# Optimization experiments

Hardware: AMD Instinct MI355X
Metric: run time of the kernel (lower is better)

Reference implementation:

```python
import jax, jax.numpy as jnp
import numpy as np

T, B, S, D, H, E, F, K = 1024, 4, 1024, 1024, 16, 8, 2048, 2


def layer_norm(x, g, b, eps=1e-5):
    mu = x.mean(-1, keepdims=True)
    var = ((x - mu) ** 2).mean(-1, keepdims=True)
    return (x - mu) * jax.lax.rsqrt(var + eps) * g + b


def mha(q_in, k_in, v_in, Wq, bq, Wk, bk, Wv, bv, Wo, bo, n_heads, mask):
    # q_in: [Lq,B,D], k_in/v_in: [Lk,B,D]
    Lq, Bb, Dd = q_in.shape
    Lk = k_in.shape[0]
    hd = Dd // n_heads
    scale = 1.0 / np.sqrt(hd)
    q = ((q_in @ Wq + bq) * scale).reshape(Lq, Bb, n_heads, hd)
    k = (k_in @ Wk + bk).reshape(Lk, Bb, n_heads, hd)
    v = (v_in @ Wv + bv).reshape(Lk, Bb, n_heads, hd)
    scores = jnp.einsum('qbhd,kbhd->bhqk', q, k)  # [B,H,Lq,Lk]
    if mask is not None:
        scores = scores + mask  # additive mask broadcast over B,H
    p = jax.nn.softmax(scores, axis=-1)
    o = jnp.einsum('bhqk,kbhd->qbhd', p, v).reshape(Lq, Bb, Dd)
    return o @ Wo + bo


def moe_ffn(x2, gate_W, W1, b1, W2, b2, top_k):
    # x2: [N,D] flattened tokens. Top-k routing: softmax over the k selected logits.
    logits = x2 @ gate_W                      # [N,E]
    top_v, top_i = jax.lax.top_k(logits, top_k)
    gk = jax.nn.softmax(top_v, axis=-1)       # [N,k]
    gates = jnp.sum(jax.nn.one_hot(top_i, logits.shape[-1], dtype=x2.dtype) * gk[..., None], axis=1)  # [N,E] sparse
    out = jnp.zeros_like(x2)
    for e in range(W1.shape[0]):  # fixed small expert count
        h = jax.nn.relu(x2 @ W1[e] + b1[e])   # [N,F]
        out = out + gates[:, e:e + 1] * (h @ W2[e] + b2[e])
    return out


def _forward(x, encoder_out, self_attn_mask,
             ln1_g, ln1_b, ln2_g, ln2_b, ln3_g, ln3_b,
             sa_Wq, sa_bq, sa_Wk, sa_bk, sa_Wv, sa_bv, sa_Wo, sa_bo,
             ca_Wq, ca_bq, ca_Wk, ca_bk, ca_Wv, ca_bv, ca_Wo, ca_bo,
             gate_W, moe_W1, moe_b1, moe_W2, moe_b2):
    # pre-LN self-attention
    res = x
    xn = layer_norm(x, ln1_g, ln1_b)
    a = mha(xn, xn, xn, sa_Wq, sa_bq, sa_Wk, sa_bk, sa_Wv, sa_bv, sa_Wo, sa_bo, H, self_attn_mask)
    x = res + a
    # pre-LN cross-attention
    res = x
    xn = layer_norm(x, ln2_g, ln2_b)
    a = mha(xn, encoder_out, encoder_out, ca_Wq, ca_bq, ca_Wk, ca_bk, ca_Wv, ca_bv, ca_Wo, ca_bo, H, None)
    x = res + a
    # pre-LN MoE FFN
    res = x
    xn = layer_norm(x, ln3_g, ln3_b)
    m = moe_ffn(xn.reshape(-1, D), gate_W, moe_W1, moe_b1, moe_W2, moe_b2, K).reshape(x.shape)
    return res + m


def setup_inputs() -> dict:
    key = jax.random.key(0)
    ks = jax.random.split(key, 20)
    w = lambda k, shp: (jax.random.normal(k, shp, jnp.float32) * 0.02)
    causal = jnp.where(jnp.arange(T)[:, None] >= jnp.arange(T)[None, :], 0.0, -1e9).astype(jnp.float32)
    return {
        'x': jax.random.normal(ks[0], (T, B, D), jnp.float32),
        'encoder_out': jax.random.normal(ks[1], (S, B, D), jnp.float32),
        'self_attn_mask': causal,
        'ln1_g': jnp.ones((D,), jnp.float32), 'ln1_b': jnp.zeros((D,), jnp.float32),
        'ln2_g': jnp.ones((D,), jnp.float32), 'ln2_b': jnp.zeros((D,), jnp.float32),
        'ln3_g': jnp.ones((D,), jnp.float32), 'ln3_b': jnp.zeros((D,), jnp.float32),
        'sa_Wq': w(ks[2], (D, D)), 'sa_bq': jnp.zeros((D,), jnp.float32),
        'sa_Wk': w(ks[3], (D, D)), 'sa_bk': jnp.zeros((D,), jnp.float32),
        'sa_Wv': w(ks[4], (D, D)), 'sa_bv': jnp.zeros((D,), jnp.float32),
        'sa_Wo': w(ks[5], (D, D)), 'sa_bo': jnp.zeros((D,), jnp.float32),
        'ca_Wq': w(ks[6], (D, D)), 'ca_bq': jnp.zeros((D,), jnp.float32),
        'ca_Wk': w(ks[7], (D, D)), 'ca_bk': jnp.zeros((D,), jnp.float32),
        'ca_Wv': w(ks[8], (D, D)), 'ca_bv': jnp.zeros((D,), jnp.float32),
        'ca_Wo': w(ks[9], (D, D)), 'ca_bo': jnp.zeros((D,), jnp.float32),
        'gate_W': w(ks[10], (D, E)),
        'moe_W1': w(ks[11], (E, D, F)), 'moe_b1': jnp.zeros((E, F), jnp.float32),
        'moe_W2': w(ks[12], (E, F, D)), 'moe_b2': jnp.zeros((E, D), jnp.float32),
    }


def reference(x, encoder_out, self_attn_mask,
              ln1_g, ln1_b, ln2_g, ln2_b, ln3_g, ln3_b,
              sa_Wq, sa_bq, sa_Wk, sa_bk, sa_Wv, sa_bv, sa_Wo, sa_bo,
              ca_Wq, ca_bq, ca_Wk, ca_bk, ca_Wv, ca_bv, ca_Wo, ca_bo,
              gate_W, moe_W1, moe_b1, moe_W2, moe_b2):
    return _forward(x, encoder_out, self_attn_mask,
                    ln1_g, ln1_b, ln2_g, ln2_b, ln3_g, ln3_b,
                    sa_Wq, sa_bq, sa_Wk, sa_bk, sa_Wv, sa_bv, sa_Wo, sa_bo,
                    ca_Wq, ca_bq, ca_Wk, ca_bk, ca_Wv, ca_bv, ca_Wo, ca_bo,
                    gate_W, moe_W1, moe_b1, moe_W2, moe_b2)
```

## Files before the change

### kernel.cpp

```cpp
#include <hip/hip_runtime.h>
#include <hip/hip_bf16.h>

typedef unsigned short u16;
typedef float f32x4 __attribute__((ext_vector_type(4)));
typedef __bf16 bf16x8 __attribute__((ext_vector_type(8)));
typedef unsigned short u16x8 __attribute__((ext_vector_type(8)));
typedef unsigned short u16x4 __attribute__((ext_vector_type(4)));

__device__ __forceinline__ u16 f2bf(float f) {
    unsigned int u = __builtin_bit_cast(unsigned int, f);
    u += 0x7fffu + ((u >> 16) & 1u);
    return (u16)(u >> 16);
}
__device__ __forceinline__ float bf2f(u16 h) {
    unsigned int u = ((unsigned int)h) << 16;
    return __builtin_bit_cast(float, u);
}
__device__ __forceinline__ f32x4 mfma_bf16(u16x8 a, u16x8 b, f32x4 c) {
    return __builtin_amdgcn_mfma_f32_16x16x32_bf16(
        __builtin_bit_cast(bf16x8, a), __builtin_bit_cast(bf16x8, b), c, 0, 0, 0);
}
__device__ __forceinline__ void gload16(const void* g, void* l) {
    __builtin_amdgcn_global_load_lds(
        (const __attribute__((address_space(1))) unsigned int*)g,
        (__attribute__((address_space(3))) unsigned int*)l, 16, 0, 0);
}
__device__ __forceinline__ int swz_bid(int hw, int nwg) {
    return (hw & 7) * (nwg >> 3) + (hw >> 3);
}

template<bool GATHER>
__device__ __forceinline__ void gemm_core(
        const u16* __restrict__ Ab, const u16* __restrict__ Bb,
        int m0, int n0, int Klen, int Ksa, int Ksb, int cnt, const int* __restrict__ idx,
        u16* lds_a, u16* lds_b, f32x4 (&acc)[4][4]) {
    const int tid = threadIdx.x;
    const int w = tid >> 6, l = tid & 63;
    const int c8 = l & 7, r8 = l >> 3;
    const int lr = l & 15, lg = l >> 4;
    const int wr = (w >> 1) * 64, wc = (w & 1) * 64;
    const int swz = (c8 ^ r8) << 4;

    const char* asrc[4];
    const char* bsrc[4];
    #pragma unroll
    for (int i = 0; i < 4; i++) {
        int row = w * 32 + i * 8 + r8;
        int gr = m0 + row; if (gr > cnt - 1) gr = cnt - 1;
        if (GATHER) gr = idx[gr];
        asrc[i] = (const char*)Ab + (size_t)gr * Ksa * 2 + swz;
        bsrc[i] = (const char*)Bb + (size_t)(n0 + row) * Ksb * 2 + swz;
    }
    for (int k0 = 0; k0 < Klen; k0 += 64) {
        __syncthreads();
        #pragma unroll
        for (int i = 0; i < 4; i++) {
            gload16(asrc[i] + (size_t)k0 * 2, lds_a + (w * 32 + i * 8) * 64);
            gload16(bsrc[i] + (size_t)k0 * 2, lds_b + (w * 32 + i * 8) * 64);
        }
        __syncthreads();
        #pragma unroll
        for (int kk = 0; kk < 2; kk++) {
            u16x8 af[4], bfr[4];
            #pragma unroll
            for (int mi = 0; mi < 4; mi++) {
                int m = wr + mi * 16 + lr;
                af[mi] = *(const u16x8*)((const char*)lds_a + m * 128 + (((kk * 4 + lg) ^ (m & 7)) << 4));
            }
            #pragma unroll
            for (int ni = 0; ni < 4; ni++) {
                int n = wc + ni * 16 + lr;
                bfr[ni] = *(const u16x8*)((const char*)lds_b + n * 128 + (((kk * 4 + lg) ^ (n & 7)) << 4));
            }
            #pragma unroll
            for (int mi = 0; mi < 4; mi++)
                #pragma unroll
                for (int ni = 0; ni < 4; ni++)
                    acc[mi][ni] = mfma_bf16(af[mi], bfr[ni], acc[mi][ni]);
        }
    }
}

struct Slab5 { const u16* a; const u16* bt; const float* bias; u16* cb; float sc; };
struct Slabs5 { Slab5 s[5]; };

template<int MODE, int NSLAB>
__global__ __launch_bounds__(256, 3) void gemm_dense(
        Slabs5 P, const float* __restrict__ extra, float* __restrict__ Cf, int K) {
    __shared__ __align__(16) u16 lds_a[128 * 64];
    __shared__ __align__(16) u16 lds_b[128 * 64];
    const int gx = NSLAB * 8;
    const int lid = swz_bid((int)blockIdx.x + gx * (int)blockIdx.y, gx * 32);
    const int bx = lid % gx, by = lid / gx;
    const int slab = (NSLAB == 1) ? 0 : (bx >> 3);
    const int n0 = ((NSLAB == 1) ? bx : (bx & 7)) * 128;
    const int m0 = by * 128;
    f32x4 acc[4][4];
    #pragma unroll
    for (int i = 0; i < 4; i++)
        #pragma unroll
        for (int j = 0; j < 4; j++) acc[i][j] = (f32x4){0.f, 0.f, 0.f, 0.f};

    gemm_core<false>(P.s[slab].a, P.s[slab].bt, m0, n0, K, K, K, 0x7fffffff, nullptr, lds_a, lds_b, acc);

    const int tid = threadIdx.x, w = tid >> 6, l = tid & 63;
    const int lr = l & 15, lg = l >> 4, wr = (w >> 1) * 64, wc = (w & 1) * 64;
    const float* bias = P.s[slab].bias;
    #pragma unroll
    for (int ni = 0; ni < 4; ni++) {
        int col = n0 + wc + ni * 16 + lr;
        float bv = bias[col];
        #pragma unroll
        for (int mi = 0; mi < 4; mi++) {
            #pragma unroll
            for (int r = 0; r < 4; r++) {
                int row = m0 + wr + mi * 16 + lg * 4 + r;
                float v = acc[mi][ni][r] + bv;
                size_t off = (size_t)row * 1024 + col;
                if (MODE == 1) Cf[off] = v + extra[off];
                else           P.s[slab].cb[off] = f2bf(v * P.s[slab].sc);
            }
        }
    }
}

__global__ __launch_bounds__(256, 3) void gemm_moe1(
        const u16* __restrict__ XNb, const u16* __restrict__ W1b, const float* __restrict__ b1,
        u16* __restrict__ HB, const int* __restrict__ eidx,
        const int* __restrict__ ecnt, const int* __restrict__ eoff) {
    __shared__ __align__(16) u16 lds_a[128 * 64];
    __shared__ __align__(16) u16 lds_b[128 * 64];
    const int lid = swz_bid((int)blockIdx.x + 16 * ((int)blockIdx.y + 32 * (int)blockIdx.z), 4096);
    const int bx = lid & 15, rem = lid >> 4;
    const int by = rem & 31, e = rem >> 5;
    const int cnt = ecnt[e];
    const int m0 = by * 128;
    if (m0 >= cnt) return;
    const int n0 = bx * 128;
    const int* idx = eidx + e * 4096;
    f32x4 acc[4][4];
    #pragma unroll
    for (int i = 0; i < 4; i++)
        #pragma unroll
        for (int j = 0; j < 4; j++) acc[i][j] = (f32x4){0.f, 0.f, 0.f, 0.f};

    gemm_core<true>(XNb, W1b + (size_t)e * 2048 * 1024, m0, n0, 1024, 1024, 1024, cnt, idx, lds_a, lds_b, acc);

    const int tid = threadIdx.x, w = tid >> 6, l = tid & 63;
    const int lr = l & 15, lg = l >> 4, wr = (w >> 1) * 64, wc = (w & 1) * 64;
    u16* H = HB + (size_t)eoff[e] * 2048;
    const float* bias = b1 + (size_t)e * 2048;
    #pragma unroll
    for (int ni = 0; ni < 4; ni++) {
        int col = n0 + wc + ni * 16 + lr;
        float bv = bias[col];
        #pragma unroll
        for (int mi = 0; mi < 4; mi++) {
            #pragma unroll
            for (int r = 0; r < 4; r++) {
                int row = m0 + wr + mi * 16 + lg * 4 + r;
                if (row < cnt)
                    H[(size_t)row * 2048 + col] = f2bf(fmaxf(acc[mi][ni][r] + bv, 0.f));
            }
        }
    }
}

__global__ __launch_bounds__(256, 3) void gemm_moe2(
        const u16* __restrict__ HB, const u16* __restrict__ W2b, const float* __restrict__ b2,
        u16* __restrict__ Y,
        const int* __restrict__ ecnt, const int* __restrict__ eoff) {
    __shared__ __align__(16) u16 lds_a[128 * 64];
    __shared__ __align__(16) u16 lds_b[128 * 64];
    const int lid = swz_bid((int)blockIdx.x + 8 * ((int)blockIdx.y + 32 * (int)blockIdx.z), 2048);
    const int bx = lid & 7, rem = lid >> 3;
    const int by = rem & 31, e = rem >> 5;
    const int cnt = ecnt[e];
    const int m0 = by * 128;
    if (m0 >= cnt) return;
    const int n0 = bx * 128;
    const u16* Ae = HB + (size_t)eoff[e] * 2048;
    f32x4 acc[4][4];
    #pragma unroll
    for (int i = 0; i < 4; i++)
        #pragma unroll
        for (int j = 0; j < 4; j++) acc[i][j] = (f32x4){0.f, 0.f, 0.f, 0.f};

    gemm_core<false>(Ae, W2b + (size_t)e * 1024 * 2048, m0, n0, 2048, 2048, 2048, cnt, nullptr, lds_a, lds_b, acc);

    const int tid = threadIdx.x, w = tid >> 6, l = tid & 63;
    const int lr = l & 15, lg = l >> 4, wr = (w >> 1) * 64, wc = (w & 1) * 64;
    const float* bias = b2 + (size_t)e * 1024;
    u16* Ye = Y + (size_t)eoff[e] * 1024;
    #pragma unroll
    for (int ni = 0; ni < 4; ni++) {
        int col = n0 + wc + ni * 16 + lr;
        float bv = bias[col];
        #pragma unroll
        for (int mi = 0; mi < 4; mi++) {
            #pragma unroll
            for (int r = 0; r < 4; r++) {
                int row = m0 + wr + mi * 16 + lg * 4 + r;
                if (row < cnt)
                    Ye[(size_t)row * 1024 + col] = f2bf(acc[mi][ni][r] + bv);
            }
        }
    }
}

__global__ void combine_kernel(const float* __restrict__ g2, const int* __restrict__ slotmap,
                               const int* __restrict__ eoff, const u16* __restrict__ Y,
                               float* __restrict__ out) {
    int t = blockIdx.x * 4 + (threadIdx.x >> 6);
    int l = threadIdx.x & 63;
    int s0 = slotmap[t * 2], s1 = slotmap[t * 2 + 1];
    float g0 = g2[t * 2], g1 = g2[t * 2 + 1];
    int r0 = eoff[s0 >> 16] + (s0 & 0xffff);
    int r1 = eoff[s1 >> 16] + (s1 & 0xffff);
    const u16* y0 = Y + (size_t)r0 * 1024 + l * 16;
    const u16* y1 = Y + (size_t)r1 * 1024 + l * 16;
    float* op = out + (size_t)t * 1024 + l * 16;
    u16x8 a0 = *(const u16x8*)y0;
    u16x8 a1 = *(const u16x8*)(y0 + 8);
    u16x8 b0 = *(const u16x8*)y1;
    u16x8 b1 = *(const u16x8*)(y1 + 8);
    f32x4 o[4];
    #pragma unroll
    for (int j = 0; j < 4; j++) o[j] = *(const f32x4*)(op + j * 4);
    #pragma unroll
    for (int j = 0; j < 4; j++) {
        o[0][j] += g0 * bf2f(a0[j])     + g1 * bf2f(b0[j]);
        o[1][j] += g0 * bf2f(a0[j + 4]) + g1 * bf2f(b0[j + 4]);
        o[2][j] += g0 * bf2f(a1[j])     + g1 * bf2f(b1[j]);
        o[3][j] += g0 * bf2f(a1[j + 4]) + g1 * bf2f(b1[j + 4]);
    }
    #pragma unroll
    for (int j = 0; j < 4; j++) *(f32x4*)(op + j * 4) = o[j];
}

template<bool F32OUT>
__global__ void ln_kernel(const float* __restrict__ X, const float* __restrict__ g,
                          const float* __restrict__ bt, u16* __restrict__ Yb,
                          float* __restrict__ Yf) {
    int row = blockIdx.x * 4 + (threadIdx.x >> 6);
    int l = threadIdx.x & 63;
    const float* x = X + (size_t)row * 1024;
    f32x4 v[4];
    float s = 0.f, s2 = 0.f;
    #pragma unroll
    for (int i = 0; i < 4; i++) {
        v[i] = *reinterpret_cast<const f32x4*>(x + i * 256 + l * 4);
        #pragma unroll
        for (int j = 0; j < 4; j++) { s += v[i][j]; s2 += v[i][j] * v[i][j]; }
    }
    #pragma unroll
    for (int m = 1; m < 64; m <<= 1) { s += __shfl_xor(s, m); s2 += __shfl_xor(s2, m); }
    float mu = s * (1.f / 1024.f);
    float var = s2 * (1.f / 1024.f) - mu * mu;
    float rs = rsqrtf(var + 1e-5f);
    #pragma unroll
    for (int i = 0; i < 4; i++) {
        f32x4 gv = *reinterpret_cast<const f32x4*>(g + i * 256 + l * 4);
        f32x4 bv = *reinterpret_cast<const f32x4*>(bt + i * 256 + l * 4);
        f32x4 o;
        u16x4 ob;
        #pragma unroll
        for (int j = 0; j < 4; j++) { o[j] = (v[i][j] - mu) * rs * gv[j] + bv[j]; ob[j] = f2bf(o[j]); }
        *reinterpret_cast<u16x4*>(Yb + (size_t)row * 1024 + i * 256 + l * 4) = ob;
        if (F32OUT) *reinterpret_cast<f32x4*>(Yf + (size_t)row * 1024 + i * 256 + l * 4) = o;
    }
}

struct Ptr8 { const float* p[8]; };
__global__ void wtrans_kernel(Ptr8 srcs, u16* __restrict__ dst, int K, int N) {
    __shared__ float t[64][65];
    const float* W = srcs.p[blockIdx.z];
    u16* Wt = dst + (size_t)blockIdx.z * K * N;
    int k0 = blockIdx.y * 64, n0 = blockIdx.x * 64;
    int tx = threadIdx.x, ty = threadIdx.y;
    #pragma unroll
    for (int i = 0; i < 8; i++) t[ty + i * 8][tx] = W[(size_t)(k0 + ty + i * 8) * N + n0 + tx];
    __syncthreads();
    #pragma unroll
    for (int i = 0; i < 8; i++) Wt[(size_t)(n0 + ty + i * 8) * K + k0 + tx] = f2bf(t[tx][ty + i * 8]);
}

__global__ void cvt_kernel(const float* __restrict__ s, u16* __restrict__ d, int n) {
    int i = ((int)blockIdx.x * 256 + (int)threadIdx.x) * 8;
    if (i >= n) return;
    f32x4 a = *reinterpret_cast<const f32x4*>(s + i);
    f32x4 b = *reinterpret_cast<const f32x4*>(s + i + 4);
    u16x8 h;
    h[0] = f2bf(a[0]); h[1] = f2bf(a[1]); h[2] = f2bf(a[2]); h[3] = f2bf(a[3]);
    h[4] = f2bf(b[0]); h[5] = f2bf(b[1]); h[6] = f2bf(b[2]); h[7] = f2bf(b[3]);
    *reinterpret_cast<u16x8*>(d + i) = h;
}

__global__ void transpose_v(const u16* __restrict__ V, u16* __restrict__ Vt) {
    __shared__ u16 tile[32][34];
    int s0 = blockIdx.x * 32;
    int d0 = blockIdx.y * 32;
    int bh = blockIdx.z;
    int b = bh >> 4, h = bh & 15;
    int tx = threadIdx.x, ty = threadIdx.y;
    #pragma unroll
    for (int i = 0; i < 4; i++) {
        int s = s0 + ty + i * 8;
        tile[ty + i * 8][tx] = V[((size_t)s * 4 + b) * 1024 + h * 64 + d0 + tx];
    }
    __syncthreads();
    #pragma unroll
    for (int i = 0; i < 4; i++) {
        int d = d0 + ty + i * 8;
        Vt[((size_t)(bh * 64 + d)) * 1024 + s0 + tx] = tile[tx][ty + i * 8];
    }
}

template<bool CAUSAL>
__global__ __launch_bounds__(256, 3) void attn_kernel(
        const u16* __restrict__ Q, const u16* __restrict__ Km,
        const u16* __restrict__ Vt, u16* __restrict__ O) {
    __shared__ __align__(16) u16 kt_lds[2][64 * 64];
    __shared__ __align__(16) u16 vt_lds[2][64 * 64];
    __shared__ __align__(16) u16 p_lds[4][16 * 68];

    const int lid = swz_bid((int)blockIdx.x, 1024);
    const int qt = lid & 15;
    const int hh = (lid >> 4) & 15;
    const int b  = lid >> 8;
    const int tid = threadIdx.x;
    const int w = tid >> 6, l = tid & 63;
    const int lr = l & 15, lg = l >> 4;
    const int c8 = l & 7, r8 = l >> 3;
    const int qb = qt * 64;

    u16x8 qf0, qf1;
    {
        const u16* qp = Q + ((size_t)(qb + w * 16 + lr) * 4 + b) * 1024 + hh * 64 + lg * 8;
        qf0 = *(const u16x8*)qp;
        qf1 = *(const u16x8*)(qp + 32);
    }
    const u16* kbase = Km + (size_t)b * 1024 + (size_t)hh * 64 + ((c8 ^ r8) << 3);
    const u16* vbase = Vt + ((size_t)(b * 16 + hh) * 64) * 1024 + ((c8 ^ r8) << 3);

    f32x4 o[4];
    #pragma unroll
    for (int ni = 0; ni < 4; ni++) o[ni] = (f32x4){0.f, 0.f, 0.f, 0.f};
    float Mr[4], Lr[4];
    #pragma unroll
    for (int r = 0; r < 4; r++) { Mr[r] = -1e30f; Lr[r] = 0.f; }

    const int nkt = CAUSAL ? (qt + 1) : 16;

    #pragma unroll
    for (int i = 0; i < 2; i++) {
        int rrow = w * 16 + i * 8 + r8;
        gload16(kbase + (size_t)rrow * 4096, &kt_lds[0][(w * 16 + i * 8) * 64]);
        gload16(vbase + (size_t)rrow * 1024, &vt_lds[0][(w * 16 + i * 8) * 64]);
    }
    __syncthreads();

    for (int kt = 0; kt < nkt; ++kt) {
        const int buf = kt & 1;
        if (kt + 1 < nkt) {
            #pragma unroll
            for (int i = 0; i < 2; i++) {
                int rrow = w * 16 + i * 8 + r8;
                gload16(kbase + (size_t)((kt + 1) * 64 + rrow) * 4096, &kt_lds[buf ^ 1][(w * 16 + i * 8) * 64]);
                gload16(vbase + (size_t)rrow * 1024 + (kt + 1) * 64, &vt_lds[buf ^ 1][(w * 16 + i * 8) * 64]);
            }
        }
        f32x4 s4[4];
        #pragma unroll
        for (int g = 0; g < 4; g++) {
            int krow = g * 16 + lr;
            const char* kl = (const char*)kt_lds[buf] + krow * 128;
            u16x8 kf0 = *(const u16x8*)(kl + ((lg ^ (krow & 7)) << 4));
            u16x8 kf1 = *(const u16x8*)(kl + (((lg + 4) ^ (krow & 7)) << 4));
            s4[g] = mfma_bf16(qf0, kf0, (f32x4){0.f, 0.f, 0.f, 0.f});
            s4[g] = mfma_bf16(qf1, kf1, s4[g]);
        }
        if (CAUSAL && kt == qt) {
            #pragma unroll
            for (int g = 0; g < 4; g++) {
                int kg = kt * 64 + g * 16 + lr;
                #pragma unroll
                for (int r = 0; r < 4; r++) {
                    int qg = qb + w * 16 + lg * 4 + r;
                    if (kg > qg) s4[g][r] = -1e30f;
                }
            }
        }
        #pragma unroll
        for (int r = 0; r < 4; r++) {
            float mx = fmaxf(fmaxf(s4[0][r], s4[1][r]), fmaxf(s4[2][r], s4[3][r]));
            mx = fmaxf(mx, __shfl_xor(mx, 1));
            mx = fmaxf(mx, __shfl_xor(mx, 2));
            mx = fmaxf(mx, __shfl_xor(mx, 4));
            mx = fmaxf(mx, __shfl_xor(mx, 8));
            float newM = fmaxf(Mr[r], mx);
            float corr = __expf(Mr[r] - newM);
            float p0 = __expf(s4[0][r] - newM);
            float p1 = __expf(s4[1][r] - newM);
            float p2 = __expf(s4[2][r] - newM);
            float p3 = __expf(s4[3][r] - newM);
            float ps = (p0 + p1) + (p2 + p3);
            ps += __shfl_xor(ps, 1); ps += __shfl_xor(ps, 2);
            ps += __shfl_xor(ps, 4); ps += __shfl_xor(ps, 8);
            Lr[r] = Lr[r] * corr + ps;
            Mr[r] = newM;
            o[0][r] *= corr; o[1][r] *= corr; o[2][r] *= corr; o[3][r] *= corr;
            int prow = lg * 4 + r;
            p_lds[w][prow * 68 + lr] = f2bf(p0);
            p_lds[w][prow * 68 + 16 + lr] = f2bf(p1);
            p_lds[w][prow * 68 + 32 + lr] = f2bf(p2);
            p_lds[w][prow * 68 + 48 + lr] = f2bf(p3);
        }
        asm volatile("s_waitcnt lgkmcnt(0)" ::: "memory");
        #pragma unroll
        for (int kk = 0; kk < 2; kk++) {
            u16x8 pf = *(const u16x8*)&p_lds[w][lr * 68 + kk * 32 + lg * 8];
            #pragma unroll
            for (int ni = 0; ni < 4; ni++) {
                int vrow = ni * 16 + lr;
                const char* vl = (const char*)vt_lds[buf] + vrow * 128;
                u16x8 vf = *(const u16x8*)(vl + (((kk * 4 + lg) ^ (vrow & 7)) << 4));
                o[ni] = mfma_bf16(pf, vf, o[ni]);
            }
        }
        __syncthreads();
    }
    #pragma unroll
    for (int ni = 0; ni < 4; ni++) {
        #pragma unroll
        for (int r = 0; r < 4; r++) {
            int row = qb + w * 16 + lg * 4 + r;
            int col = ni * 16 + lr;
            O[((size_t)row * 4 + b) * 1024 + hh * 64 + col] = f2bf(o[ni][r] / Lr[r]);
        }
    }
}

__global__ void gate_kernel(const float* __restrict__ XN, const float* __restrict__ GW,
                            float* __restrict__ g2, int* __restrict__ top2) {
    int t = blockIdx.x * 4 + (threadIdx.x >> 6);
    int l = threadIdx.x & 63;
    const float* x = XN + (size_t)t * 1024 + l * 16;
    double p[8] = {0, 0, 0, 0, 0, 0, 0, 0};
    #pragma unroll
    for (int i = 0; i < 16; i++) {
        float xc = x[i];
        const float* gw = GW + (size_t)(l * 16 + i) * 8;
        #pragma unroll
        for (int e = 0; e < 8; e++) p[e] += (double)xc * (double)gw[e];
    }
    #pragma unroll
    for (int e = 0; e < 8; e++) {
        #pragma unroll
        for (int m = 1; m < 64; m <<= 1) p[e] += __shfl_xor(p[e], m);
    }
    if (l == 0) {
        int i0 = 0; double v0 = p[0];
        #pragma unroll
        for (int e = 1; e < 8; e++) if (p[e] > v0) { v0 = p[e]; i0 = e; }
        int i1 = -1; double v1 = -1e300;
        #pragma unroll
        for (int e = 0; e < 8; e++) if (e != i0 && p[e] > v1) { v1 = p[e]; i1 = e; }
        float ex = __expf((float)(v1 - v0));
        float ga = 1.f / (1.f + ex);
        float gb = ex * ga;
        g2[t * 2] = ga; g2[t * 2 + 1] = gb;
        top2[t] = i0 | (i1 << 8);
    }
}

__global__ void build_lists(const int* __restrict__ top2, int* __restrict__ eidx,
                            int* __restrict__ ecnt, int* __restrict__ slotmap) {
    const int e = blockIdx.x;
    const int tid = threadIdx.x;
    const int w = tid >> 6, l = tid & 63;
    __shared__ int wcnt[4];
    int base = 0;
    for (int c = 0; c < 4096; c += 256) {
        int tok = c + tid;
        int t2 = top2[tok];
        bool pf = ((t2 & 0xff) == e);
        bool ps = (((t2 >> 8) & 0xff) == e);
        bool pred = pf || ps;
        unsigned long long mask = __ballot(pred);
        if (l == 0) wcnt[w] = __popcll(mask);
        __syncthreads();
        int wb = base;
        for (int i = 0; i < w; i++) wb += wcnt[i];
        int pos = __popcll(mask & ((1ull << l) - 1ull));
        if (pred) {
            eidx[e * 4096 + wb + pos] = tok;
            slotmap[tok * 2 + (pf ? 0 : 1)] = (e << 16) | (wb + pos);
        }
        base += wcnt[0] + wcnt[1] + wcnt[2] + wcnt[3];
        __syncthreads();
    }
    if (tid == 0) ecnt[e] = base;
}

__global__ void scan_kernel(const int* __restrict__ ecnt, int* __restrict__ eoff) {
    if (threadIdx.x == 0) {
        int s = 0;
        for (int e = 0; e < 8; e++) { eoff[e] = s; s += ecnt[e]; }
    }
}

extern "C" void kernel_launch(void* const* d_in, const int* in_sizes, int n_in,
                              void* d_out, int out_size, void* d_ws, size_t ws_size,
                              hipStream_t stream) {
    const float* x    = (const float*)d_in[0];
    const float* enc  = (const float*)d_in[1];
    const float* ln1g = (const float*)d_in[3];
    const float* ln1b = (const float*)d_in[4];
    const float* ln2g = (const float*)d_in[5];
    const float* ln2b = (const float*)d_in[6];
    const float* ln3g = (const float*)d_in[7];
    const float* ln3b = (const float*)d_in[8];
    const float* saWq = (const float*)d_in[9];  const float* sabq = (const float*)d_in[10];
    const float* saWk = (const float*)d_in[11]; const float* sabk = (const float*)d_in[12];
    const float* saWv = (const float*)d_in[13]; const float* sabv = (const float*)d_in[14];
    const float* saWo = (const float*)d_in[15]; const float* sabo = (const float*)d_in[16];
    const float* caWq = (const float*)d_in[17]; const float* cabq = (const float*)d_in[18];
    const float* caWk = (const float*)d_in[19]; const float* cabk = (const float*)d_in[20];
    const float* caWv = (const float*)d_in[21]; const float* cabv = (const float*)d_in[22];
    const float* caWo = (const float*)d_in[23]; const float* cabo = (const float*)d_in[24];
    const float* gateW = (const float*)d_in[25];
    const float* W1 = (const float*)d_in[26]; const float* b1 = (const float*)d_in[27];
    const float* W2 = (const float*)d_in[28]; const float* b2 = (const float*)d_in[29];
    float* out = (float*)d_out;
    char* W = (char*)d_ws;

    const size_t MB = 1ull << 20;
    u16*   Wattn = (u16*)(W);
    u16*   Qb    = (u16*)(W + 16 * MB);
    u16*   Kb    = (u16*)(W + 24 * MB);
    u16*   Vb    = (u16*)(W + 32 * MB);
    u16*   VTb   = (u16*)(W + 40 * MB);
    u16*   ATb   = (u16*)(W + 48 * MB);
    u16*   encb  = (u16*)(W + 56 * MB);
    u16*   XNb   = (u16*)(W + 64 * MB);
    float* X1    = (float*)(W + 72 * MB);
    u16*   K2b   = (u16*)(W + 88 * MB);
    u16*   V2b   = (u16*)(W + 96 * MB);
    u16*   HB    = (u16*)(W + 88 * MB);
    u16*   W1b   = (u16*)(W);
    u16*   W2b   = (u16*)(W + 32 * MB);
    u16*   Yc    = (u16*)(W);
    float* g2    = (float*)(W + 120 * MB);
    int*   eidx  = (int*)(W + 120 * MB + 128 * 1024);
    int*   ecnt  = (int*)(W + 120 * MB + 256 * 1024);
    int*   eoff  = ecnt + 16;
    int*   top2  = (int*)(W + 120 * MB + 272 * 1024);
    int*   slotmap = (int*)(W + 120 * MB + 320 * 1024);

    dim3 bw(64, 8);
    const float SC = 0.125f;

    {
        Ptr8 p; p.p[0]=saWq; p.p[1]=saWk; p.p[2]=saWv; p.p[3]=saWo;
                p.p[4]=caWq; p.p[5]=caWk; p.p[6]=caWv; p.p[7]=caWo;
        wtrans_kernel<<<dim3(16, 16, 8), bw, 0, stream>>>(p, Wattn, 1024, 1024);
    }
    cvt_kernel<<<2048, 256, 0, stream>>>(enc, encb, 4096 * 1024);

    ln_kernel<false><<<1024, 256, 0, stream>>>(x, ln1g, ln1b, XNb, nullptr);
    {
        Slabs5 P;
        P.s[0] = {XNb,  Wattn,               sabq, Qb,  SC };
        P.s[1] = {XNb,  Wattn + 1 * 1048576, sabk, Kb,  1.f};
        P.s[2] = {XNb,  Wattn + 2 * 1048576, sabv, Vb,  1.f};
        P.s[3] = {encb, Wattn + 5 * 1048576, cabk, K2b, 1.f};
        P.s[4] = {encb, Wattn + 6 * 1048576, cabv, V2b, 1.f};
        gemm_dense<2, 5><<<dim3(40, 32), 256, 0, stream>>>(P, nullptr, nullptr, 1024);
    }
    transpose_v<<<dim3(32, 2, 64), dim3(32, 8), 0, stream>>>(Vb, VTb);
    attn_kernel<true><<<1024, 256, 0, stream>>>(Qb, Kb, VTb, ATb);
    {
        Slabs5 P; P.s[0] = {ATb, Wattn + 3 * 1048576, sabo, nullptr, 1.f};
        gemm_dense<1, 1><<<dim3(8, 32), 256, 0, stream>>>(P, x, X1, 1024);
    }

    ln_kernel<false><<<1024, 256, 0, stream>>>(X1, ln2g, ln2b, XNb, nullptr);
    {
        Slabs5 P; P.s[0] = {XNb, Wattn + 4 * 1048576, cabq, Qb, SC};
        gemm_dense<2, 1><<<dim3(8, 32), 256, 0, stream>>>(P, nullptr, nullptr, 1024);
    }
    transpose_v<<<dim3(32, 2, 64), dim3(32, 8), 0, stream>>>(V2b, VTb);
    attn_kernel<false><<<1024, 256, 0, stream>>>(Qb, K2b, VTb, ATb);
    {
        Slabs5 P; P.s[0] = {ATb, Wattn + 7 * 1048576, cabo, nullptr, 1.f};
        gemm_dense<1, 1><<<dim3(8, 32), 256, 0, stream>>>(P, X1, out, 1024);
    }

    {
        Ptr8 p1; for (int e = 0; e < 8; e++) p1.p[e] = W1 + (size_t)e * 1024 * 2048;
        wtrans_kernel<<<dim3(32, 16, 8), bw, 0, stream>>>(p1, W1b, 1024, 2048);
        Ptr8 p2; for (int e = 0; e < 8; e++) p2.p[e] = W2 + (size_t)e * 2048 * 1024;
        wtrans_kernel<<<dim3(16, 32, 8), bw, 0, stream>>>(p2, W2b, 2048, 1024);
    }
    ln_kernel<true><<<1024, 256, 0, stream>>>(out, ln3g, ln3b, XNb, X1);
    gate_kernel<<<1024, 256, 0, stream>>>(X1, gateW, g2, top2);
    build_lists<<<8, 256, 0, stream>>>(top2, eidx, ecnt, slotmap);
    scan_kernel<<<1, 64, 0, stream>>>(ecnt, eoff);
    gemm_moe1<<<dim3(16, 32, 8), 256, 0, stream>>>(XNb, W1b, b1, HB, eidx, ecnt, eoff);
    gemm_moe2<<<dim3(8, 32, 8), 256, 0, stream>>>(HB, W2b, b2, Yc, ecnt, eoff);
    combine_kernel<<<1024, 256, 0, stream>>>(g2, slotmap, eoff, Yc, out);
}
```

Measured before the change: 498.5 us.

## Single-buffer attention K/V tiles, raise occupancy, add lazy softmax rescale

Replaces the double-buffered K/V LDS tiles in the attention kernel with a single buffer that is loaded synchronously at the top of each iteration. Launch bounds go from 3 to 6 blocks per CU to raise occupancy, relying on other resident blocks to hide load latency in place of in-block prefetch. It also adds a lazy online-softmax rescale: the running max and the output/sum correction are only updated when some row's new max exceeds the old one by more than 8. This saves exponentials and multiplies in the common case, at the cost of a wave-wide vote and some headroom against overflow of the exponentials.

```diff
diff --git a/kernel.cpp b/kernel.cpp
--- a/kernel.cpp
+++ b/kernel.cpp
@@ -317,11 +317,11 @@
 }
 
 template<bool CAUSAL>
-__global__ __launch_bounds__(256, 3) void attn_kernel(
+__global__ __launch_bounds__(256, 6) void attn_kernel(
         const u16* __restrict__ Q, const u16* __restrict__ Km,
         const u16* __restrict__ Vt, u16* __restrict__ O) {
-    __shared__ __align__(16) u16 kt_lds[2][64 * 64];
-    __shared__ __align__(16) u16 vt_lds[2][64 * 64];
+    __shared__ __align__(16) u16 kt_lds[64 * 64];
+    __shared__ __align__(16) u16 vt_lds[64 * 64];
     __shared__ __align__(16) u16 p_lds[4][16 * 68];
 
     const int lid = swz_bid((int)blockIdx.x, 1024);
@@ -352,29 +352,21 @@
 
     const int nkt = CAUSAL ? (qt + 1) : 16;
 
-    #pragma unroll
-    for (int i = 0; i < 2; i++) {
-        int rrow = w * 16 + i * 8 + r8;
-        gload16(kbase + (size_t)rrow * 4096, &kt_lds[0][(w * 16 + i * 8) * 64]);
-        gload16(vbase + (size_t)rrow * 1024, &vt_lds[0][(w * 16 + i * 8) * 64]);
-    }
-    __syncthreads();
-
     for (int kt = 0; kt < nkt; ++kt) {
-        const int buf = kt & 1;
-        if (kt + 1 < nkt) {
-            #pragma unroll
-            for (int i = 0; i < 2; i++) {
-                int rrow = w * 16 + i * 8 + r8;
-                gload16(kbase + (size_t)((kt + 1) * 64 + rrow) * 4096, &kt_lds[buf ^ 1][(w * 16 + i * 8) * 64]);
-                gload16(vbase + (size_t)rrow * 1024 + (kt + 1) * 64, &vt_lds[buf ^ 1][(w * 16 + i * 8) * 64]);
-            }
-        }
+        __syncthreads();
+        #pragma unroll
+        for (int i = 0; i < 2; i++) {
+            int rrow = w * 16 + i * 8 + r8;
+            gload16(kbase + (size_t)(kt * 64 + rrow) * 4096, &kt_lds[(w * 16 + i * 8) * 64]);
+            gload16(vbase + (size_t)rrow * 1024 + kt * 64, &vt_lds[(w * 16 + i * 8) * 64]);
+        }
+        __syncthreads();
+
         f32x4 s4[4];
         #pragma unroll
         for (int g = 0; g < 4; g++) {
             int krow = g * 16 + lr;
-            const char* kl = (const char*)kt_lds[buf] + krow * 128;
+            const char* kl = (const char*)kt_lds + krow * 128;
             u16x8 kf0 = *(const u16x8*)(kl + ((lg ^ (krow & 7)) << 4));
             u16x8 kf1 = *(const u16x8*)(kl + (((lg + 4) ^ (krow & 7)) << 4));
             s4[g] = mfma_bf16(qf0, kf0, (f32x4){0.f, 0.f, 0.f, 0.f});
@@ -391,25 +383,35 @@
                 }
             }
         }
+        float mx[4];
         #pragma unroll
         for (int r = 0; r < 4; r++) {
-            float mx = fmaxf(fmaxf(s4[0][r], s4[1][r]), fmaxf(s4[2][r], s4[3][r]));
-            mx = fmaxf(mx, __shfl_xor(mx, 1));
-            mx = fmaxf(mx, __shfl_xor(mx, 2));
-            mx = fmaxf(mx, __shfl_xor(mx, 4));
-            mx = fmaxf(mx, __shfl_xor(mx, 8));
-            float newM = fmaxf(Mr[r], mx);
-            float corr = __expf(Mr[r] - newM);
-            float p0 = __expf(s4[0][r] - newM);
-            float p1 = __expf(s4[1][r] - newM);
-            float p2 = __expf(s4[2][r] - newM);
-            float p3 = __expf(s4[3][r] - newM);
+            float m_ = fmaxf(fmaxf(s4[0][r], s4[1][r]), fmaxf(s4[2][r], s4[3][r]));
+            m_ = fmaxf(m_, __shfl_xor(m_, 1));
+            m_ = fmaxf(m_, __shfl_xor(m_, 2));
+            m_ = fmaxf(m_, __shfl_xor(m_, 4));
+            m_ = fmaxf(m_, __shfl_xor(m_, 8));
+            mx[r] = m_;
+        }
+        bool fast = __all((mx[0] <= Mr[0] + 8.f) && (mx[1] <= Mr[1] + 8.f) &&
+                          (mx[2] <= Mr[2] + 8.f) && (mx[3] <= Mr[3] + 8.f));
+        #pragma unroll
+        for (int r = 0; r < 4; r++) {
+            if (!fast) {
+                float newM = fmaxf(Mr[r], mx[r]);
+                float corr = __expf(Mr[r] - newM);
+                Lr[r] *= corr;
+                o[0][r] *= corr; o[1][r] *= corr; o[2][r] *= corr; o[3][r] *= corr;
+                Mr[r] = newM;
+            }
+            float p0 = __expf(s4[0][r] - Mr[r]);
+            float p1 = __expf(s4[1][r] - Mr[r]);
+            float p2 = __expf(s4[2][r] - Mr[r]);
+            float p3 = __expf(s4[3][r] - Mr[r]);
             float ps = (p0 + p1) + (p2 + p3);
             ps += __shfl_xor(ps, 1); ps += __shfl_xor(ps, 2);
             ps += __shfl_xor(ps, 4); ps += __shfl_xor(ps, 8);
-            Lr[r] = Lr[r] * corr + ps;
-            Mr[r] = newM;
-            o[0][r] *= corr; o[1][r] *= corr; o[2][r] *= corr; o[3][r] *= corr;
+            Lr[r] += ps;
             int prow = lg * 4 + r;
             p_lds[w][prow * 68 + lr] = f2bf(p0);
             p_lds[w][prow * 68 + 16 + lr] = f2bf(p1);
@@ -423,12 +425,11 @@
             #pragma unroll
             for (int ni = 0; ni < 4; ni++) {
                 int vrow = ni * 16 + lr;
-                const char* vl = (const char*)vt_lds[buf] + vrow * 128;
+                const char* vl = (const char*)vt_lds + vrow * 128;
                 u16x8 vf = *(const u16x8*)(vl + (((kk * 4 + lg) ^ (vrow & 7)) << 4));
                 o[ni] = mfma_bf16(pf, vf, o[ni]);
             }
         }
-        __syncthreads();
     }
     #pragma unroll
     for (int ni = 0; ni < 4; ni++) {
```

After: 568.4 us. 1.14x slower.
